# Kernel optimization log

Hardware: AMD Instinct MI355X
Metric: run time of the kernel (lower is better)

## Reference

```python
import jax, jax.numpy as jnp
import numpy as np

N = 12288
E = 393216
IN = 64
OUT = 64
EPS = 1e-8


def setup_inputs() -> dict:
    key = jax.random.key(0)
    k1, k2, k3, k4, k5 = jax.random.split(key, 5)
    x = jax.random.normal(k1, (N, IN), dtype=jnp.float32)
    edge_index = jax.random.randint(k2, (2, E), 0, N, dtype=jnp.int32)
    W_self = jax.random.normal(k3, (OUT, IN), dtype=jnp.float32) / np.sqrt(IN)
    W_neigh = jax.random.normal(k4, (OUT, IN), dtype=jnp.float32) / np.sqrt(IN)
    bound = 1.0 / np.sqrt(IN)
    bias = jax.random.uniform(k5, (OUT,), dtype=jnp.float32, minval=-bound, maxval=bound)
    return {"x": x, "edge_index": edge_index, "W_self": W_self, "W_neigh": W_neigh, "bias": bias}


def _proj_norm(p):
    # normalize feature part, keep homogeneous coordinate
    feat = p[..., :-1]
    norm = jnp.linalg.norm(feat, axis=-1, keepdims=True)
    return jnp.concatenate([feat / (norm + EPS), p[..., -1:]], axis=-1)


def _proj_transform(x, W):
    # x: [N, in+1], W: [out, in] -> [N, out+1]
    feat = x[..., :-1] @ W.T
    return _proj_norm(jnp.concatenate([feat, x[..., -1:]], axis=-1))


def _proj_average(points, weights):
    # points: [K, ..., D], weights: [K]
    avg = jnp.einsum('k,k...->...', weights, points)
    return _proj_norm(avg)


def _forward(x, edge_index, W_self, W_neigh, bias):
    xh = jnp.concatenate([x, jnp.ones_like(x[..., :1])], axis=-1)  # [N, in+1]
    self_trans = _proj_transform(xh, W_self)  # [N, out+1]

    # --- aggregate_neighbors ---
    row, col = edge_index[0], edge_index[1]
    all_nodes = _proj_transform(xh, W_neigh)  # [N, out+1]
    n = xh.shape[0]
    adj = jnp.zeros((n, n), jnp.float32).at[row, col].set(1.0) + jnp.eye(n, dtype=jnp.float32)
    # per-edge cross-ratio weight (symmetric in src/dst)
    xf = xh[..., :-1]
    ps, pd = xf[row], xf[col]  # [E, in]
    cos = jnp.sum(ps * pd, axis=-1) / (
        jnp.linalg.norm(ps, axis=-1) * jnp.linalg.norm(pd, axis=-1) + EPS)
    w = jnp.clip((cos + 1.0) * 0.5, 0.1, 0.9)  # [E]
    adj = adj.at[row, col].set(w).at[col, row].set(w)
    adj = adj / (adj.sum(axis=1, keepdims=True) + EPS)
    neigh_trans = _proj_norm(adj @ all_nodes)  # [N, out+1]

    # --- combine self and neighbor, then bias ---
    out = _proj_average(jnp.stack([self_trans, neigh_trans]),
                        jnp.array([0.5, 0.5], jnp.float32))
    bp = jnp.concatenate([bias, jnp.ones_like(bias[:1])])
    bp = bp / jnp.linalg.norm(bp)
    out = _proj_average(jnp.stack([out, jnp.broadcast_to(bp, out.shape)]),
                        jnp.array([0.9, 0.1], jnp.float32))
    feat = out[..., :-1]
    return feat / (jnp.linalg.norm(feat, axis=-1, keepdims=True) + EPS)


def reference(x, edge_index, W_self, W_neigh, bias):
    return _forward(x, edge_index, W_self, W_neigh, bias)
```

## Files before the change

### kernel.cpp

```cpp
#include <hip/hip_runtime.h>
#include <math.h>

#define N_NODES 12288
#define N_EDGES 393216
#define EPS 1e-8f

#define NB 1024
#define NPB 12
#define NXCD 8
#define NSUB (NB * NXCD)
#define CAP_SUB 256
#define NSLOT 128
#define BMW 384

__device__ __forceinline__ float wave_sum(float v) {
    #pragma unroll
    for (int off = 32; off; off >>= 1) v += __shfl_xor(v, off);
    return v;
}

__global__ __launch_bounds__(256) void phase1_kernel(
    const float* __restrict__ x, const float* __restrict__ Wself,
    const float* __restrict__ Wneigh,
    float* __restrict__ s_norm, float* __restrict__ anf) {
    __shared__ float Wl[2 * 64 * 65];
    const int tid = threadIdx.x;
    #pragma unroll
    for (int v = 0; v < 4; ++v) {
        const int idx4 = v * 256 + tid;
        const int o = idx4 >> 4, k4 = (idx4 & 15) << 2;
        const float4 a = *(const float4*)&Wself[idx4 << 2];
        Wl[o * 65 + k4 + 0] = a.x; Wl[o * 65 + k4 + 1] = a.y;
        Wl[o * 65 + k4 + 2] = a.z; Wl[o * 65 + k4 + 3] = a.w;
        const float4 b = *(const float4*)&Wneigh[idx4 << 2];
        float* W2 = &Wl[64 * 65];
        W2[o * 65 + k4 + 0] = b.x; W2[o * 65 + k4 + 1] = b.y;
        W2[o * 65 + k4 + 2] = b.z; W2[o * 65 + k4 + 3] = b.w;
    }
    __syncthreads();

    const int o = tid & 63;
    const int wq = tid >> 6;
    const int i0 = (blockIdx.x * 4 + wq) * 4;
    const float* xr0 = &x[(size_t)(i0 + 0) * 64];
    const float* xr1 = &x[(size_t)(i0 + 1) * 64];
    const float* xr2 = &x[(size_t)(i0 + 2) * 64];
    const float* xr3 = &x[(size_t)(i0 + 3) * 64];
    const float* Ws = &Wl[o * 65];
    const float* Wn = &Wl[64 * 65 + o * 65];

    float ys0 = 0.f, ys1 = 0.f, ys2 = 0.f, ys3 = 0.f;
    float yn0 = 0.f, yn1 = 0.f, yn2 = 0.f, yn3 = 0.f;
    #pragma unroll
    for (int t = 0; t < 16; ++t) {
        const int kb = 4 * t;
        const float4 a0 = *(const float4*)&xr0[kb];
        const float4 a1 = *(const float4*)&xr1[kb];
        const float4 a2 = *(const float4*)&xr2[kb];
        const float4 a3 = *(const float4*)&xr3[kb];
        #pragma unroll
        for (int u = 0; u < 4; ++u) {
            const float ws = Ws[kb + u];
            const float wn = Wn[kb + u];
            const float e0 = u == 0 ? a0.x : u == 1 ? a0.y : u == 2 ? a0.z : a0.w;
            const float e1 = u == 0 ? a1.x : u == 1 ? a1.y : u == 2 ? a1.z : a1.w;
            const float e2 = u == 0 ? a2.x : u == 1 ? a2.y : u == 2 ? a2.z : a2.w;
            const float e3 = u == 0 ? a3.x : u == 1 ? a3.y : u == 2 ? a3.z : a3.w;
            ys0 = fmaf(e0, ws, ys0); yn0 = fmaf(e0, wn, yn0);
            ys1 = fmaf(e1, ws, ys1); yn1 = fmaf(e1, wn, yn1);
            ys2 = fmaf(e2, ws, ys2); yn2 = fmaf(e2, wn, yn2);
            ys3 = fmaf(e3, ws, ys3); yn3 = fmaf(e3, wn, yn3);
        }
    }

    const float ns0 = sqrtf(wave_sum(ys0 * ys0));
    const float ns1 = sqrtf(wave_sum(ys1 * ys1));
    const float ns2 = sqrtf(wave_sum(ys2 * ys2));
    const float ns3 = sqrtf(wave_sum(ys3 * ys3));
    const float nn0 = sqrtf(wave_sum(yn0 * yn0));
    const float nn1 = sqrtf(wave_sum(yn1 * yn1));
    const float nn2 = sqrtf(wave_sum(yn2 * yn2));
    const float nn3 = sqrtf(wave_sum(yn3 * yn3));

    s_norm[(size_t)(i0 + 0) * 64 + o] = ys0 / (ns0 + EPS);
    s_norm[(size_t)(i0 + 1) * 64 + o] = ys1 / (ns1 + EPS);
    s_norm[(size_t)(i0 + 2) * 64 + o] = ys2 / (ns2 + EPS);
    s_norm[(size_t)(i0 + 3) * 64 + o] = ys3 / (ns3 + EPS);
    anf[(size_t)(i0 + 0) * 64 + o] = yn0 / (nn0 + EPS);
    anf[(size_t)(i0 + 1) * 64 + o] = yn1 / (nn1 + EPS);
    anf[(size_t)(i0 + 2) * 64 + o] = yn2 / (nn2 + EPS);
    anf[(size_t)(i0 + 3) * 64 + o] = yn3 / (nn3 + EPS);
}

__global__ __launch_bounds__(256) void edge_bin_kernel(
    const float* __restrict__ x, const int* __restrict__ ei,
    int* __restrict__ subcnt, int2* __restrict__ buf) {
    const int lane = threadIdx.x & 63;
    const int j = lane & 7;
    const int wave = blockIdx.x * 4 + (threadIdx.x >> 6);
    const int e = wave * 8 + (lane >> 3);

    const int r = ei[e];
    const int c = ei[N_EDGES + e];

    const size_t rb = (size_t)r * 64 + j * 8;
    const size_t cb = (size_t)c * 64 + j * 8;
    const float4 xr0 = *(const float4*)&x[rb];
    const float4 xr1 = *(const float4*)&x[rb + 4];
    const float4 xc0 = *(const float4*)&x[cb];
    const float4 xc1 = *(const float4*)&x[cb + 4];

    float p = xr0.x*xc0.x + xr0.y*xc0.y + xr0.z*xc0.z + xr0.w*xc0.w
            + xr1.x*xc1.x + xr1.y*xc1.y + xr1.z*xc1.z + xr1.w*xc1.w;
    float nr = xr0.x*xr0.x + xr0.y*xr0.y + xr0.z*xr0.z + xr0.w*xr0.w
             + xr1.x*xr1.x + xr1.y*xr1.y + xr1.z*xr1.z + xr1.w*xr1.w;
    float nc = xc0.x*xc0.x + xc0.y*xc0.y + xc0.z*xc0.z + xc0.w*xc0.w
             + xc1.x*xc1.x + xc1.y*xc1.y + xc1.z*xc1.z + xc1.w*xc1.w;
    #pragma unroll
    for (int off = 1; off < 8; off <<= 1) {
        p  += __shfl_xor(p,  off);
        nr += __shfl_xor(nr, off);
        nc += __shfl_xor(nc, off);
    }

    const float cosv = p / (sqrtf(nr) * sqrtf(nc) + EPS);
    float w = fminf(fmaxf((cosv + 1.0f) * 0.5f, 0.1f), 0.9f);
    const float wv = (r == c) ? (w - 1.0f) : w;
    const int wbits = __float_as_int(wv);

    int xcc;
    asm volatile("s_getreg_b32 %0, hwreg(20, 0, 4)" : "=s"(xcc));
    xcc &= 7;

    if (j < 2) {
        const int dest = j ? c : r;
        const int col  = j ? r : c;
        const int sub = (dest / NPB) * NXCD + xcc;
        const int s = atomicAdd(&subcnt[sub], 1);
        if (s < CAP_SUB)
            buf[(size_t)sub * CAP_SUB + s] = make_int2((dest << 14) | col, wbits);
    }
}

__global__ __launch_bounds__(256) void bin_gather_kernel(
    const int* __restrict__ subcnt, const int2* __restrict__ buf,
    const float* __restrict__ anf, const float* __restrict__ s_norm,
    const float* __restrict__ bias, float* __restrict__ out) {
    __shared__ int2 csr[NPB][NSLOT];
    __shared__ unsigned bm[NPB * BMW];
    __shared__ int cnt[NPB];
    const int tid = threadIdx.x;
    const int lane = tid & 63;
    const int w4 = tid >> 6;
    const int bin = blockIdx.x;
    const int node0 = bin * NPB;

    for (int t = tid; t < NPB * BMW; t += 256) bm[t] = 0u;
    if (tid < NPB) cnt[tid] = 0;
    __syncthreads();

    for (int xc = 0; xc < NXCD; ++xc) {
        const int sub = bin * NXCD + xc;
        const int n = min(subcnt[sub], CAP_SUB);
        const int2* seg = &buf[(size_t)sub * CAP_SUB];
        for (int t = tid; t < n; t += 256) {
            const int2 rec = seg[t];
            const int dest = rec.x >> 14;
            const int col  = rec.x & 16383;
            const int l = dest - node0;
            const unsigned bit = 1u << (col & 31);
            const unsigned old = atomicOr(&bm[l * BMW + (col >> 5)], bit);
            if (!(old & bit)) {
                const int s = atomicAdd(&cnt[l], 1);
                if (s < NSLOT) csr[l][s] = make_int2(col, rec.y);
            }
        }
    }
    __syncthreads();

    const float bd = bias[lane];
    const float nb = sqrtf(wave_sum(bd * bd) + 1.0f);
    const float bterm = 0.1f * (bd / nb);

    #pragma unroll 1
    for (int q = 0; q < 3; ++q) {
        const int l = w4 * 3 + q;
        const int i = node0 + l;
        const int d = min(cnt[l], NSLOT);

        float acc = anf[(size_t)i * 64 + lane];
        #pragma unroll 4
        for (int k = 0; k < d; ++k) {
            const int2 ent = csr[l][k];
            acc = fmaf(__int_as_float(ent.y), anf[(size_t)ent.x * 64 + lane], acc);
        }
        float Sp = 0.f;
        if (lane < d)      Sp += __int_as_float(csr[l][lane].y);
        if (lane + 64 < d) Sp += __int_as_float(csr[l][lane + 64].y);
        const float S = 1.0f + wave_sum(Sp);

        const float v = acc / (S + EPS);
        const float nv = sqrtf(wave_sum(v * v));
        const float nf = v / (nv + EPS);

        const float s = s_norm[(size_t)i * 64 + lane];
        const float h = 0.5f * (s + nf);
        const float nh = sqrtf(wave_sum(h * h));
        const float hf = h / (nh + EPS);

        const float g = 0.9f * hf + bterm;
        const float ng = sqrtf(wave_sum(g * g));
        const float gf = g / (ng + EPS);

        const float rho = ng / (ng + EPS);
        out[(size_t)i * 64 + lane] = gf / (rho + EPS);
    }
}

extern "C" void kernel_launch(void* const* d_in, const int* in_sizes, int n_in,
                              void* d_out, int out_size, void* d_ws, size_t ws_size,
                              hipStream_t stream) {
    const float* x      = (const float*)d_in[0];
    const int*   ei     = (const int*)  d_in[1];
    const float* Wself  = (const float*)d_in[2];
    const float* Wneigh = (const float*)d_in[3];
    const float* bias   = (const float*)d_in[4];
    float* out = (float*)d_out;

    const size_t ROW_BYTES = (size_t)N_NODES * 64 * sizeof(float);
    char* ws = (char*)d_ws;
    int*  subcnt = (int*)ws;   ws += (size_t)NSUB * sizeof(int);
    int2* buf    = (int2*)ws;  ws += (size_t)NSUB * CAP_SUB * sizeof(int2);
    float* s_norm = (float*)ws; ws += ROW_BYTES;
    float* anf    = (float*)ws; ws += ROW_BYTES;

    hipMemsetAsync(subcnt, 0, (size_t)NSUB * sizeof(int), stream);

    edge_bin_kernel<<<N_EDGES / 8 / 4, 256, 0, stream>>>(x, ei, subcnt, buf);

    phase1_kernel<<<768, 256, 0, stream>>>(x, Wself, Wneigh, s_norm, anf);

    bin_gather_kernel<<<NB, 256, 0, stream>>>(subcnt, buf, anf, s_norm,
                                              bias, out);
}
```

Baseline: 136.8 us.

## Fuse edge binning, projection and gather into one cooperative kernel with grid sync

Merges the three kernel launches (edge binning, node projection, bin gather) into a single cooperative kernel of 1024 blocks. Edge work is grid-strided, each block projects its own 12 nodes, and a grid-wide sync separates the scatter phase from the gather phase. The goal is to remove launch overhead and inter-kernel gaps, at the cost of a grid barrier and a fixed occupancy requirement of 4 blocks per CU. The old three-kernel path is kept as a fallback when that occupancy is not available.

```diff
diff --git a/kernel.cpp b/kernel.cpp
--- a/kernel.cpp
+++ b/kernel.cpp
@@ -1,5 +1,8 @@
 #include <hip/hip_runtime.h>
+#include <hip/hip_cooperative_groups.h>
 #include <math.h>
+
+namespace cg = cooperative_groups;
 
 #define N_NODES 12288
 #define N_EDGES 393216
@@ -12,11 +15,197 @@
 #define CAP_SUB 256
 #define NSLOT 128
 #define BMW 384
+#define SM_FLOATS (2 * 64 * 65)
 
 __device__ __forceinline__ float wave_sum(float v) {
     #pragma unroll
     for (int off = 32; off; off >>= 1) v += __shfl_xor(v, off);
     return v;
+}
+
+__global__ __launch_bounds__(256, 4) void fused_kernel(
+    const float* __restrict__ x, const int* __restrict__ ei,
+    const float* __restrict__ Wself, const float* __restrict__ Wneigh,
+    const float* __restrict__ bias,
+    int* __restrict__ subcnt, int2* __restrict__ buf,
+    float* __restrict__ s_norm, float* __restrict__ anf,
+    float* __restrict__ out) {
+    __shared__ float smraw[SM_FLOATS];
+    const int tid = threadIdx.x;
+    const int lane = tid & 63;
+    const int wq = tid >> 6;
+    const int bid = blockIdx.x;
+
+    float* Wl = smraw;
+    #pragma unroll
+    for (int v = 0; v < 4; ++v) {
+        const int idx4 = v * 256 + tid;
+        const int o = idx4 >> 4, k4 = (idx4 & 15) << 2;
+        const float4 a = *(const float4*)&Wself[idx4 << 2];
+        Wl[o * 65 + k4 + 0] = a.x; Wl[o * 65 + k4 + 1] = a.y;
+        Wl[o * 65 + k4 + 2] = a.z; Wl[o * 65 + k4 + 3] = a.w;
+        const float4 b = *(const float4*)&Wneigh[idx4 << 2];
+        float* W2 = &Wl[64 * 65];
+        W2[o * 65 + k4 + 0] = b.x; W2[o * 65 + k4 + 1] = b.y;
+        W2[o * 65 + k4 + 2] = b.z; W2[o * 65 + k4 + 3] = b.w;
+    }
+    __syncthreads();
+
+    int xcc;
+    asm volatile("s_getreg_b32 %0, hwreg(20, 0, 4)" : "=s"(xcc));
+    xcc &= 7;
+    const int j = lane & 7;
+    const int gw = bid * 4 + wq;
+    for (int g = gw; g < N_EDGES / 8; g += NB * 4) {
+        const int e = g * 8 + (lane >> 3);
+        const int r = ei[e];
+        const int c = ei[N_EDGES + e];
+
+        const size_t rb = (size_t)r * 64 + j * 8;
+        const size_t cb = (size_t)c * 64 + j * 8;
+        const float4 xr0 = *(const float4*)&x[rb];
+        const float4 xr1 = *(const float4*)&x[rb + 4];
+        const float4 xc0 = *(const float4*)&x[cb];
+        const float4 xc1 = *(const float4*)&x[cb + 4];
+
+        float p = xr0.x*xc0.x + xr0.y*xc0.y + xr0.z*xc0.z + xr0.w*xc0.w
+                + xr1.x*xc1.x + xr1.y*xc1.y + xr1.z*xc1.z + xr1.w*xc1.w;
+        float nr = xr0.x*xr0.x + xr0.y*xr0.y + xr0.z*xr0.z + xr0.w*xr0.w
+                 + xr1.x*xr1.x + xr1.y*xr1.y + xr1.z*xr1.z + xr1.w*xr1.w;
+        float nc = xc0.x*xc0.x + xc0.y*xc0.y + xc0.z*xc0.z + xc0.w*xc0.w
+                 + xc1.x*xc1.x + xc1.y*xc1.y + xc1.z*xc1.z + xc1.w*xc1.w;
+        #pragma unroll
+        for (int off = 1; off < 8; off <<= 1) {
+            p  += __shfl_xor(p,  off);
+            nr += __shfl_xor(nr, off);
+            nc += __shfl_xor(nc, off);
+        }
+
+        const float cosv = p / (sqrtf(nr) * sqrtf(nc) + EPS);
+        float w = fminf(fmaxf((cosv + 1.0f) * 0.5f, 0.1f), 0.9f);
+        const float wv = (r == c) ? (w - 1.0f) : w;
+        const int wbits = __float_as_int(wv);
+
+        if (j < 2) {
+            const int dest = j ? c : r;
+            const int col  = j ? r : c;
+            const int sub = (dest / NPB) * NXCD + xcc;
+            const int s = atomicAdd(&subcnt[sub], 1);
+            if (s < CAP_SUB)
+                buf[(size_t)sub * CAP_SUB + s] = make_int2((dest << 14) | col, wbits);
+        }
+    }
+
+    {
+        const int i0 = bid * NPB + wq * 3;
+        const float* xr0 = &x[(size_t)(i0 + 0) * 64];
+        const float* xr1 = &x[(size_t)(i0 + 1) * 64];
+        const float* xr2 = &x[(size_t)(i0 + 2) * 64];
+        const int o = lane;
+        const float* Ws = &Wl[o * 65];
+        const float* Wn = &Wl[64 * 65 + o * 65];
+
+        float ys0 = 0.f, ys1 = 0.f, ys2 = 0.f;
+        float yn0 = 0.f, yn1 = 0.f, yn2 = 0.f;
+        #pragma unroll
+        for (int t = 0; t < 16; ++t) {
+            const int kb = 4 * t;
+            const float4 a0 = *(const float4*)&xr0[kb];
+            const float4 a1 = *(const float4*)&xr1[kb];
+            const float4 a2 = *(const float4*)&xr2[kb];
+            #pragma unroll
+            for (int u = 0; u < 4; ++u) {
+                const float ws = Ws[kb + u];
+                const float wn = Wn[kb + u];
+                const float e0 = u == 0 ? a0.x : u == 1 ? a0.y : u == 2 ? a0.z : a0.w;
+                const float e1 = u == 0 ? a1.x : u == 1 ? a1.y : u == 2 ? a1.z : a1.w;
+                const float e2 = u == 0 ? a2.x : u == 1 ? a2.y : u == 2 ? a2.z : a2.w;
+                ys0 = fmaf(e0, ws, ys0); yn0 = fmaf(e0, wn, yn0);
+                ys1 = fmaf(e1, ws, ys1); yn1 = fmaf(e1, wn, yn1);
+                ys2 = fmaf(e2, ws, ys2); yn2 = fmaf(e2, wn, yn2);
+            }
+        }
+        const float ns0 = sqrtf(wave_sum(ys0 * ys0));
+        const float ns1 = sqrtf(wave_sum(ys1 * ys1));
+        const float ns2 = sqrtf(wave_sum(ys2 * ys2));
+        const float nn0 = sqrtf(wave_sum(yn0 * yn0));
+        const float nn1 = sqrtf(wave_sum(yn1 * yn1));
+        const float nn2 = sqrtf(wave_sum(yn2 * yn2));
+        s_norm[(size_t)(i0 + 0) * 64 + o] = ys0 / (ns0 + EPS);
+        s_norm[(size_t)(i0 + 1) * 64 + o] = ys1 / (ns1 + EPS);
+        s_norm[(size_t)(i0 + 2) * 64 + o] = ys2 / (ns2 + EPS);
+        anf[(size_t)(i0 + 0) * 64 + o] = yn0 / (nn0 + EPS);
+        anf[(size_t)(i0 + 1) * 64 + o] = yn1 / (nn1 + EPS);
+        anf[(size_t)(i0 + 2) * 64 + o] = yn2 / (nn2 + EPS);
+    }
+
+    __threadfence();
+    cg::this_grid().sync();
+
+    int2* csr    = (int2*)smraw;
+    unsigned* bm = (unsigned*)(smraw + NPB * NSLOT * 2);
+    int* cnt     = (int*)(smraw + NPB * NSLOT * 2 + NPB * BMW);
+
+    for (int t = tid; t < NPB * BMW; t += 256) bm[t] = 0u;
+    if (tid < NPB) cnt[tid] = 0;
+    __syncthreads();
+
+    for (int xc = 0; xc < NXCD; ++xc) {
+        const int sub = bid * NXCD + xc;
+        const int n = min(subcnt[sub], CAP_SUB);
+        const int2* seg = &buf[(size_t)sub * CAP_SUB];
+        for (int t = tid; t < n; t += 256) {
+            const int2 rec = seg[t];
+            const int dest = rec.x >> 14;
+            const int col  = rec.x & 16383;
+            const int l = dest - bid * NPB;
+            const unsigned bit = 1u << (col & 31);
+            const unsigned old = atomicOr(&bm[l * BMW + (col >> 5)], bit);
+            if (!(old & bit)) {
+                const int s = atomicAdd(&cnt[l], 1);
+                if (s < NSLOT) csr[l * NSLOT + s] = make_int2(col, rec.y);
+            }
+        }
+    }
+    __syncthreads();
+
+    const float bd = bias[lane];
+    const float nb = sqrtf(wave_sum(bd * bd) + 1.0f);
+    const float bterm = 0.1f * (bd / nb);
+
+    #pragma unroll 1
+    for (int q = 0; q < 3; ++q) {
+        const int l = wq * 3 + q;
+        const int i = bid * NPB + l;
+        const int d = min(cnt[l], NSLOT);
+
+        float acc = anf[(size_t)i * 64 + lane];
+        #pragma unroll 4
+        for (int k = 0; k < d; ++k) {
+            const int2 ent = csr[l * NSLOT + k];
+            acc = fmaf(__int_as_float(ent.y), anf[(size_t)ent.x * 64 + lane], acc);
+        }
+        float Sp = 0.f;
+        if (lane < d)      Sp += __int_as_float(csr[l * NSLOT + lane].y);
+        if (lane + 64 < d) Sp += __int_as_float(csr[l * NSLOT + lane + 64].y);
+        const float S = 1.0f + wave_sum(Sp);
+
+        const float v = acc / (S + EPS);
+        const float nv = sqrtf(wave_sum(v * v));
+        const float nf = v / (nv + EPS);
+
+        const float s = s_norm[(size_t)i * 64 + lane];
+        const float h = 0.5f * (s + nf);
+        const float nh = sqrtf(wave_sum(h * h));
+        const float hf = h / (nh + EPS);
+
+        const float g = 0.9f * hf + bterm;
+        const float ng = sqrtf(wave_sum(g * g));
+        const float gf = g / (ng + EPS);
+
+        const float rho = ng / (ng + EPS);
+        out[(size_t)i * 64 + lane] = gf / (rho + EPS);
+    }
 }
 
 __global__ __launch_bounds__(256) void phase1_kernel(
@@ -38,7 +227,6 @@
         W2[o * 65 + k4 + 2] = b.z; W2[o * 65 + k4 + 3] = b.w;
     }
     __syncthreads();
-
     const int o = tid & 63;
     const int wq = tid >> 6;
     const int i0 = (blockIdx.x * 4 + wq) * 4;
@@ -48,7 +236,6 @@
     const float* xr3 = &x[(size_t)(i0 + 3) * 64];
     const float* Ws = &Wl[o * 65];
     const float* Wn = &Wl[64 * 65 + o * 65];
-
     float ys0 = 0.f, ys1 = 0.f, ys2 = 0.f, ys3 = 0.f;
     float yn0 = 0.f, yn1 = 0.f, yn2 = 0.f, yn3 = 0.f;
     #pragma unroll
@@ -72,7 +259,6 @@
             ys3 = fmaf(e3, ws, ys3); yn3 = fmaf(e3, wn, yn3);
         }
     }
-
     const float ns0 = sqrtf(wave_sum(ys0 * ys0));
     const float ns1 = sqrtf(wave_sum(ys1 * ys1));
     const float ns2 = sqrtf(wave_sum(ys2 * ys2));
@@ -81,7 +267,6 @@
     const float nn1 = sqrtf(wave_sum(yn1 * yn1));
     const float nn2 = sqrtf(wave_sum(yn2 * yn2));
     const float nn3 = sqrtf(wave_sum(yn3 * yn3));
-
     s_norm[(size_t)(i0 + 0) * 64 + o] = ys0 / (ns0 + EPS);
     s_norm[(size_t)(i0 + 1) * 64 + o] = ys1 / (ns1 + EPS);
     s_norm[(size_t)(i0 + 2) * 64 + o] = ys2 / (ns2 + EPS);
@@ -99,17 +284,14 @@
     const int j = lane & 7;
     const int wave = blockIdx.x * 4 + (threadIdx.x >> 6);
     const int e = wave * 8 + (lane >> 3);
-
     const int r = ei[e];
     const int c = ei[N_EDGES + e];
-
     const size_t rb = (size_t)r * 64 + j * 8;
     const size_t cb = (size_t)c * 64 + j * 8;
     const float4 xr0 = *(const float4*)&x[rb];
     const float4 xr1 = *(const float4*)&x[rb + 4];
     const float4 xc0 = *(const float4*)&x[cb];
     const float4 xc1 = *(const float4*)&x[cb + 4];
-
     float p = xr0.x*xc0.x + xr0.y*xc0.y + xr0.z*xc0.z + xr0.w*xc0.w
             + xr1.x*xc1.x + xr1.y*xc1.y + xr1.z*xc1.z + xr1.w*xc1.w;
     float nr = xr0.x*xr0.x + xr0.y*xr0.y + xr0.z*xr0.z + xr0.w*xr0.w
@@ -122,16 +304,13 @@
         nr += __shfl_xor(nr, off);
         nc += __shfl_xor(nc, off);
     }
-
     const float cosv = p / (sqrtf(nr) * sqrtf(nc) + EPS);
     float w = fminf(fmaxf((cosv + 1.0f) * 0.5f, 0.1f), 0.9f);
     const float wv = (r == c) ? (w - 1.0f) : w;
     const int wbits = __float_as_int(wv);
-
     int xcc;
     asm volatile("s_getreg_b32 %0, hwreg(20, 0, 4)" : "=s"(xcc));
     xcc &= 7;
-
     if (j < 2) {
         const int dest = j ? c : r;
         const int col  = j ? r : c;
@@ -154,11 +333,9 @@
     const int w4 = tid >> 6;
     const int bin = blockIdx.x;
     const int node0 = bin * NPB;
-
     for (int t = tid; t < NPB * BMW; t += 256) bm[t] = 0u;
     if (tid < NPB) cnt[tid] = 0;
     __syncthreads();
-
     for (int xc = 0; xc < NXCD; ++xc) {
         const int sub = bin * NXCD + xc;
         const int n = min(subcnt[sub], CAP_SUB);
@@ -177,17 +354,14 @@
         }
     }
     __syncthreads();
-
     const float bd = bias[lane];
     const float nb = sqrtf(wave_sum(bd * bd) + 1.0f);
     const float bterm = 0.1f * (bd / nb);
-
     #pragma unroll 1
     for (int q = 0; q < 3; ++q) {
         const int l = w4 * 3 + q;
         const int i = node0 + l;
         const int d = min(cnt[l], NSLOT);
-
         float acc = anf[(size_t)i * 64 + lane];
         #pragma unroll 4
         for (int k = 0; k < d; ++k) {
@@ -198,20 +372,16 @@
         if (lane < d)      Sp += __int_as_float(csr[l][lane].y);
         if (lane + 64 < d) Sp += __int_as_float(csr[l][lane + 64].y);
         const float S = 1.0f + wave_sum(Sp);
-
         const float v = acc / (S + EPS);
         const float nv = sqrtf(wave_sum(v * v));
         const float nf = v / (nv + EPS);
-
         const float s = s_norm[(size_t)i * 64 + lane];
         const float h = 0.5f * (s + nf);
         const float nh = sqrtf(wave_sum(h * h));
         const float hf = h / (nh + EPS);
-
         const float g = 0.9f * hf + bterm;
         const float ng = sqrtf(wave_sum(g * g));
         const float gf = g / (ng + EPS);
-
         const float rho = ng / (ng + EPS);
         out[(size_t)i * 64 + lane] = gf / (rho + EPS);
     }
@@ -229,17 +399,27 @@
 
     const size_t ROW_BYTES = (size_t)N_NODES * 64 * sizeof(float);
     char* ws = (char*)d_ws;
-    int*  subcnt = (int*)ws;   ws += (size_t)NSUB * sizeof(int);
-    int2* buf    = (int2*)ws;  ws += (size_t)NSUB * CAP_SUB * sizeof(int2);
+    int*  subcnt = (int*)ws;    ws += (size_t)NSUB * sizeof(int);
+    int2* buf    = (int2*)ws;   ws += (size_t)NSUB * CAP_SUB * sizeof(int2);
     float* s_norm = (float*)ws; ws += ROW_BYTES;
     float* anf    = (float*)ws; ws += ROW_BYTES;
 
     hipMemsetAsync(subcnt, 0, (size_t)NSUB * sizeof(int), stream);
 
-    edge_bin_kernel<<<N_EDGES / 8 / 4, 256, 0, stream>>>(x, ei, subcnt, buf);
-
-    phase1_kernel<<<768, 256, 0, stream>>>(x, Wself, Wneigh, s_norm, anf);
-
-    bin_gather_kernel<<<NB, 256, 0, stream>>>(subcnt, buf, anf, s_norm,
-                                              bias, out);
-}
+    int maxb = 0;
+    hipError_t st = hipOccupancyMaxActiveBlocksPerMultiprocessor(
+        &maxb, reinterpret_cast<const void*>(fused_kernel), 256, 0);
+
+    if (st == hipSuccess && maxb >= 4) {
+        void* args[] = {(void*)&x, (void*)&ei, (void*)&Wself, (void*)&Wneigh,
+                        (void*)&bias, (void*)&subcnt, (void*)&buf,
+                        (void*)&s_norm, (void*)&anf, (void*)&out};
+        hipLaunchCooperativeKernel(reinterpret_cast<const void*>(fused_kernel),
+                                   dim3(NB), dim3(256), args, 0, stream);
+    } else {
+        edge_bin_kernel<<<N_EDGES / 8 / 4, 256, 0, stream>>>(x, ei, subcnt, buf);
+        phase1_kernel<<<768, 256, 0, stream>>>(x, Wself, Wneigh, s_norm, anf);
+        bin_gather_kernel<<<NB, 256, 0, stream>>>(subcnt, buf, anf, s_norm,
+                                                  bias, out);
+    }
+}
```

After: 137.5 us. No clear change (+0.6%).
